# Kernel optimization log

Hardware: AMD Instinct MI355X
Metric: run time of the kernel (lower is better)

The kernel has to match this reference:

```python
import jax, jax.numpy as jnp
import numpy as np

N = 100000      # nodes
E = 1600000     # edges (before self-loops)
F_IN = 16       # num_node_features
HID = 16        # hid
HEADS = 4       # in_head == out_head
B = 64          # num graphs
G = 16          # num_global_features
NEG_SLOPE = 0.2


def gat_conv(x, src, dst, W, a_src, a_dst, b, concat):
    """PyG-style GATConv. x:[N,F], W:[F,H*C], a_src/a_dst:[H,C], b:[H*C] or [C]."""
    n = x.shape[0]
    H, C = a_src.shape
    h = (x @ W).reshape(n, H, C)                       # [N,H,C]
    alpha_s = (h * a_src).sum(-1)                      # [N,H]
    alpha_d = (h * a_dst).sum(-1)                      # [N,H]
    e = jax.nn.leaky_relu(alpha_s[src] + alpha_d[dst], NEG_SLOPE)  # [E',H]
    # segment softmax over destination nodes (stable; max is grad-free)
    m = jax.lax.stop_gradient(jax.ops.segment_max(e, dst, num_segments=n))
    ex = jnp.exp(e - m[dst])
    denom = jax.ops.segment_sum(ex, dst, num_segments=n)
    alpha = ex / (denom[dst] + 1e-16)                  # [E',H]
    out = jax.ops.segment_sum(h[src] * alpha[:, :, None], dst, num_segments=n)  # [N,H,C]
    out = out.reshape(n, H * C) if concat else out.mean(axis=1)
    return out + b


def setup_inputs() -> dict:
    key = jax.random.key(0)
    ks = jax.random.split(key, 24)
    s = 0.1
    inp = {
        "x": jax.random.normal(ks[0], (N, F_IN), jnp.float32),
        "stats": jax.random.normal(ks[1], (B, G), jnp.float32),
        # conv1: F_IN -> HID, heads=HEADS, concat=True
        "W1": jax.random.normal(ks[2], (F_IN, HEADS * HID), jnp.float32) * s,
        "a1s": jax.random.normal(ks[3], (HEADS, HID), jnp.float32) * s,
        "a1d": jax.random.normal(ks[4], (HEADS, HID), jnp.float32) * s,
        "b1": jnp.zeros((HEADS * HID,), jnp.float32),
        # conv2: HID*HEADS -> HID, heads=HEADS, concat=False
        "W2": jax.random.normal(ks[5], (HEADS * HID, HEADS * HID), jnp.float32) * s,
        "a2s": jax.random.normal(ks[6], (HEADS, HID), jnp.float32) * s,
        "a2d": jax.random.normal(ks[7], (HEADS, HID), jnp.float32) * s,
        "b2": jnp.zeros((HID,), jnp.float32),
        # conv3: HID -> HID, heads=HEADS, concat=False
        "W3": jax.random.normal(ks[8], (HID, HEADS * HID), jnp.float32) * s,
        "a3s": jax.random.normal(ks[9], (HEADS, HID), jnp.float32) * s,
        "a3d": jax.random.normal(ks[10], (HEADS, HID), jnp.float32) * s,
        "b3": jnp.zeros((HID,), jnp.float32),
        # MLP head
        "fw1": jax.random.normal(ks[11], (HID + G, 32), jnp.float32) * s,
        "fb1": jnp.zeros((32,), jnp.float32),
        "fw2": jax.random.normal(ks[12], (32, 16), jnp.float32) * s,
        "fb2": jnp.zeros((16,), jnp.float32),
        "fw3": jax.random.normal(ks[13], (16, 1), jnp.float32) * s,
        "fb3": jnp.zeros((1,), jnp.float32),
        "edge_index": jax.random.randint(ks[14], (2, E), 0, N, jnp.int64),
        "batch": jnp.sort(jax.random.randint(ks[15], (N,), 0, B, jnp.int64)),
    }
    return inp


def reference(x, stats, W1, a1s, a1d, b1, W2, a2s, a2d, b2, W3, a3s, a3d, b3,
              fw1, fb1, fw2, fb2, fw3, fb3, edge_index, batch):
    n = x.shape[0]
    loops = jnp.arange(n, dtype=edge_index.dtype)
    src = jnp.concatenate([edge_index[0], loops])  # add_self_loops=True (PyG default)
    dst = jnp.concatenate([edge_index[1], loops])
    h = jax.nn.elu(gat_conv(x, src, dst, W1, a1s, a1d, b1, True))
    h = jax.nn.elu(gat_conv(h, src, dst, W2, a2s, a2d, b2, False))
    h = gat_conv(h, src, dst, W3, a3s, a3d, b3, False)
    nb = stats.shape[0]
    pooled = jax.ops.segment_sum(h, batch, num_segments=nb)
    counts = jax.ops.segment_sum(jnp.ones((n,), h.dtype), batch, num_segments=nb)
    pooled = pooled / jnp.maximum(counts, 1.0)[:, None]   # global_mean_pool
    z = jnp.concatenate([pooled, stats], axis=1)
    z = jax.nn.relu(z @ fw1 + fb1)
    z = jax.nn.relu(z @ fw2 + fb2)
    return z @ fw3 + fb3
```

## Files before the change

kernel.cpp:

```cpp
#include <hip/hip_runtime.h>
#include <hip/hip_bf16.h>
#include <hip/hip_fp16.h>

#define NNODES 100000
#define NEDGES 1600000
#define NHEADS 4
#define NHID   16
#define NB     64
#define NG     16
#define POOL_BLOCKS 256
#define POOL_SLOTS (NB * NG + NB)

#define BKT_SHIFT 7
#define NPB 128
#define NBKT ((NNODES + NPB - 1) / NPB)
#define BCAP 4096
#define SCAT_BLOCKS 256
#define NL1_BLOCKS 2048

typedef float vf2 __attribute__((ext_vector_type(2)));

__device__ __forceinline__ float leaky02(float v) {
    return v > 0.0f ? v : 0.2f * v;
}

__device__ __forceinline__ unsigned char cvt_fp8(float a) {
    int r = __builtin_amdgcn_cvt_pk_fp8_f32(a, a, 0, false);
    return (unsigned char)(r & 0xFF);
}

__device__ __forceinline__ float4 loadQ4(const unsigned char* p) {
    int u = *(const int*)p;
    vf2 lo = __builtin_amdgcn_cvt_pk_f32_fp8(u, false);
    vf2 hi = __builtin_amdgcn_cvt_pk_f32_fp8(u, true);
    return make_float4(lo.x, lo.y, hi.x, hi.y);
}

__device__ __forceinline__ void storeH4(__half* p, float4 v) {
    __half2 a = __floats2half2_rn(v.x, v.y);
    __half2 b = __floats2half2_rn(v.z, v.w);
    uint2 raw;
    raw.x = *reinterpret_cast<unsigned*>(&a);
    raw.y = *reinterpret_cast<unsigned*>(&b);
    *(uint2*)p = raw;
}

template <int FIN>
__device__ __forceinline__ void nl_body_f32(const float* __restrict__ X,
                                            const float* __restrict__ W,
                                            const float* __restrict__ a_s,
                                            const float* __restrict__ a_d,
                                            unsigned char* __restrict__ H,
                                            float* __restrict__ AS,
                                            float* __restrict__ AD, int n,
                                            int wave0, int nwaves, int lane) {
    int head = lane >> 4;
    float w[FIN];
#pragma unroll
    for (int k = 0; k < FIN; ++k) w[k] = W[k * 64 + lane];
    float asl = a_s[lane], adl = a_d[lane];

    for (int i = wave0; i < n; i += nwaves) {
        const float* __restrict__ xr = X + (size_t)i * FIN;
        float acc = 0.0f;
#pragma unroll
        for (int k = 0; k < FIN; ++k) acc += xr[k] * w[k];
        H[(size_t)i * 64 + lane] = cvt_fp8(acc);
        float s1 = acc * asl, s2 = acc * adl;
#pragma unroll
        for (int off = 1; off < 16; off <<= 1) {
            s1 += __shfl_xor(s1, off);
            s2 += __shfl_xor(s2, off);
        }
        if ((lane & 15) == 0) {
            AS[(size_t)i * 4 + head] = s1;
            AD[(size_t)i * 4 + head] = s2;
        }
    }
}

template <int FIN>
__global__ void node_linear3(const float* __restrict__ X,
                             const float* __restrict__ W,
                             const float* __restrict__ a_s,
                             const float* __restrict__ a_d,
                             unsigned char* __restrict__ H,
                             float* __restrict__ AS,
                             float* __restrict__ AD, int n) {
    int lane = threadIdx.x & 63;
    int wave = __builtin_amdgcn_readfirstlane(
        (int)((blockIdx.x * blockDim.x + threadIdx.x) >> 6));
    int nwaves = (gridDim.x * blockDim.x) >> 6;
    nl_body_f32<FIN>(X, W, a_s, a_d, H, AS, AD, n, wave, nwaves, lane);
}

template <int FIN>
__global__ void node_linear3h(const unsigned* __restrict__ X,
                              const float* __restrict__ W,
                              const float* __restrict__ a_s,
                              const float* __restrict__ a_d,
                              unsigned char* __restrict__ H,
                              float* __restrict__ AS,
                              float* __restrict__ AD, int n) {
    int lane = threadIdx.x & 63;
    int head = lane >> 4;
    int wave = __builtin_amdgcn_readfirstlane(
        (int)((blockIdx.x * blockDim.x + threadIdx.x) >> 6));
    int nwaves = (gridDim.x * blockDim.x) >> 6;

    float w[FIN];
#pragma unroll
    for (int k = 0; k < FIN; ++k) w[k] = W[k * 64 + lane];
    float asl = a_s[lane], adl = a_d[lane];

    for (int i = wave; i < n; i += nwaves) {
        const unsigned* __restrict__ xr = X + (size_t)i * (FIN / 2);
        float acc = 0.0f;
#pragma unroll
        for (int k = 0; k < FIN / 2; ++k) {
            unsigned u = xr[k];
            __half2 hh = *reinterpret_cast<const __half2*>(&u);
            float2 f = __half22float2(hh);
            acc += f.x * w[2 * k] + f.y * w[2 * k + 1];
        }
        H[(size_t)i * 64 + lane] = cvt_fp8(acc);
        float s1 = acc * asl, s2 = acc * adl;
#pragma unroll
        for (int off = 1; off < 16; off <<= 1) {
            s1 += __shfl_xor(s1, off);
            s2 += __shfl_xor(s2, off);
        }
        if ((lane & 15) == 0) {
            AS[(size_t)i * 4 + head] = s1;
            AD[(size_t)i * 4 + head] = s2;
        }
    }
}

__global__ void scatter_nl1(const int* __restrict__ src,
                            const int* __restrict__ dst,
                            int* __restrict__ bucketCnt,
                            unsigned int* __restrict__ pairs, int ne,
                            const float* __restrict__ X,
                            const float* __restrict__ W,
                            const float* __restrict__ a_s,
                            const float* __restrict__ a_d,
                            unsigned char* __restrict__ H,
                            float* __restrict__ AS,
                            float* __restrict__ AD, int n) {
    __shared__ int hist[NBKT];
    __shared__ int base[NBKT];
    int tid = threadIdx.x;

    if (blockIdx.x >= SCAT_BLOCKS) {
        int lane = tid & 63;
        int wave = __builtin_amdgcn_readfirstlane(
            (int)(((blockIdx.x - SCAT_BLOCKS) * blockDim.x + tid) >> 6));
        int nwaves = (NL1_BLOCKS * 256) >> 6;
        nl_body_f32<16>(X, W, a_s, a_d, H, AS, AD, n, wave, nwaves, lane);
        return;
    }

    for (int i = tid; i < NBKT; i += 256) hist[i] = 0;
    __syncthreads();

    int chunk = (ne + SCAT_BLOCKS - 1) / SCAT_BLOCKS;
    int beg = blockIdx.x * chunk;
    int end = min(beg + chunk, ne);

    for (int e0 = beg; e0 < end; e0 += 1024) {
        int d[4];
#pragma unroll
        for (int q = 0; q < 4; ++q) {
            int e = e0 + q * 256 + tid;
            d[q] = (e < end) ? dst[e] : -1;
        }
#pragma unroll
        for (int q = 0; q < 4; ++q)
            if (d[q] >= 0) atomicAdd(&hist[d[q] >> BKT_SHIFT], 1);
    }
    __syncthreads();

    for (int i = tid; i < NBKT; i += 256) {
        int h = hist[i];
        base[i] = h ? atomicAdd(&bucketCnt[i], h) : 0;
        hist[i] = 0;
    }
    __syncthreads();

    for (int e0 = beg; e0 < end; e0 += 1024) {
        int d[4], s[4];
#pragma unroll
        for (int q = 0; q < 4; ++q) {
            int e = e0 + q * 256 + tid;
            d[q] = (e < end) ? dst[e] : -1;
            s[q] = (e < end) ? src[e] : 0;
        }
        int r[4], bkt[4];
#pragma unroll
        for (int q = 0; q < 4; ++q) {
            if (d[q] >= 0) {
                bkt[q] = d[q] >> BKT_SHIFT;
                r[q] = base[bkt[q]] + atomicAdd(&hist[bkt[q]], 1);
            }
        }
#pragma unroll
        for (int q = 0; q < 4; ++q) {
            if (d[q] >= 0 && r[q] < BCAP)
                pairs[(size_t)bkt[q] * BCAP + r[q]] =
                    (unsigned)s[q] | ((unsigned)(d[q] & (NPB - 1)) << 20);
        }
    }
}

__global__ void bucket_sort(const unsigned int* __restrict__ pairs,
                            const int* __restrict__ bucketCnt,
                            int* __restrict__ srcs,
                            int* __restrict__ indptr, int n) {
    __shared__ int hist[NPB];
    __shared__ int offl[NPB];
    __shared__ int cur[NPB];
    __shared__ int red[256];
    __shared__ int lsrc[BCAP];
    int bkt = blockIdx.x;
    int t = threadIdx.x;
    int cnt = min(bucketCnt[bkt], BCAP);

    int partial = 0;
    for (int j = t; j < bkt; j += 256) partial += min(bucketCnt[j], BCAP);
    red[t] = partial;
    if (t < NPB) hist[t] = 0;
    __syncthreads();
    for (int s = 128; s > 0; s >>= 1) {
        if (t < s) red[t] += red[t + s];
        __syncthreads();
    }
    int boff = red[0];
    if (bkt == NBKT - 1 && t == 0) indptr[n] = boff + cnt;

    const unsigned int* __restrict__ p = pairs + (size_t)bkt * BCAP;
    unsigned int v[BCAP / 256];
#pragma unroll
    for (int i = 0; i < BCAP / 256; ++i) {
        int e = i * 256 + t;
        v[i] = 0u;
        if (e < cnt) {
            v[i] = p[e];
            atomicAdd(&hist[v[i] >> 20], 1);
        }
    }
    __syncthreads();
    if (t < NPB) offl[t] = hist[t];
    __syncthreads();
    for (int off = 1; off < NPB; off <<= 1) {
        int x = 0;
        if (t < NPB && t >= off) x = offl[t - off];
        __syncthreads();
        if (t < NPB && t >= off) offl[t] += x;
        __syncthreads();
    }
    if (t < NPB) {
        int ex = offl[t] - hist[t];
        cur[t] = ex;
        int node = bkt * NPB + t;
        if (node < n) indptr[node] = boff + ex;
    }
    __syncthreads();
#pragma unroll
    for (int i = 0; i < BCAP / 256; ++i) {
        int e = i * 256 + t;
        if (e < cnt) {
            int r = atomicAdd(&cur[v[i] >> 20], 1);
            lsrc[r] = (int)(v[i] & 0xFFFFFu);
        }
    }
    __syncthreads();
    for (int e = t; e < cnt; e += 256) srcs[boff + e] = lsrc[e];
}

template <int MODE, typename TOUT>
__global__ void gat_pull3(const unsigned char* __restrict__ H,
                          const float* __restrict__ AS,
                          const float* __restrict__ AD,
                          const int* __restrict__ indptr,
                          const int* __restrict__ srcs,
                          const float* __restrict__ bias,
                          TOUT* __restrict__ out, int n) {
    int lane = threadIdx.x & 63;
    int grp  = lane >> 4;
    int sl   = lane & 15;
    int head = sl >> 2;
    int wave = (blockIdx.x * blockDim.x + threadIdx.x) >> 6;
    int nwaves = (gridDim.x * blockDim.x) >> 6;

    for (int d0 = wave * 4; d0 < n; d0 += nwaves * 4) {
        int d = d0 + grp;
        if (d < n) {
            float ad  = AD[(size_t)d * 4 + head];
            float asd = AS[(size_t)d * 4 + head];
            float t0 = asd + ad;
            float wself = __expf(t0 > 0.f ? t0 : 0.2f * t0);
            float den = wself;
            float4 h4s = loadQ4(H + (size_t)d * 64 + sl * 4);
            float4 acc = {wself * h4s.x, wself * h4s.y,
                          wself * h4s.z, wself * h4s.w};

            int beg = indptr[d], end = indptr[d + 1];
            for (int e0 = beg; e0 < end; e0 += 16) {
                int cnt = min(16, end - e0);
                int myS = (sl < cnt) ? srcs[e0 + sl] : 0;
                int j = 0;
                for (; j + 4 <= cnt; j += 4) {
                    int s[4]; float a[4]; float4 h4[4];
#pragma unroll
                    for (int q = 0; q < 4; ++q)
                        s[q] = __shfl(myS, (grp << 4) + j + q);
#pragma unroll
                    for (int q = 0; q < 4; ++q)
                        a[q] = AS[(size_t)s[q] * 4 + head];
#pragma unroll
                    for (int q = 0; q < 4; ++q)
                        h4[q] = loadQ4(H + (size_t)s[q] * 64 + sl * 4);
#pragma unroll
                    for (int q = 0; q < 4; ++q) {
                        float t = a[q] + ad;
                        float w = __expf(t > 0.f ? t : 0.2f * t);
                        den += w;
                        acc.x += w * h4[q].x; acc.y += w * h4[q].y;
                        acc.z += w * h4[q].z; acc.w += w * h4[q].w;
                    }
                }
                for (; j < cnt; ++j) {
                    int s = __shfl(myS, (grp << 4) + j);
                    float t = AS[(size_t)s * 4 + head] + ad;
                    float w = __expf(t > 0.f ? t : 0.2f * t);
                    den += w;
                    float4 h4 = loadQ4(H + (size_t)s * 64 + sl * 4);
                    acc.x += w * h4.x; acc.y += w * h4.y;
                    acc.z += w * h4.z; acc.w += w * h4.w;
                }
            }
            float inv = 1.0f / (den + 1e-16f);
            float4 v = {acc.x * inv, acc.y * inv, acc.z * inv, acc.w * inv};
            if (MODE == 0) {
                float4 b4 = *(const float4*)(bias + sl * 4);
                v.x += b4.x; v.y += b4.y; v.z += b4.z; v.w += b4.w;
                v.x = v.x > 0.f ? v.x : __expf(v.x) - 1.f;
                v.y = v.y > 0.f ? v.y : __expf(v.y) - 1.f;
                v.z = v.z > 0.f ? v.z : __expf(v.z) - 1.f;
                v.w = v.w > 0.f ? v.w : __expf(v.w) - 1.f;
                storeH4((__half*)out + (size_t)d * 64 + sl * 4, v);
            } else {
#pragma unroll
                for (int off = 4; off <= 8; off <<= 1) {
                    v.x += __shfl_xor(v.x, off);
                    v.y += __shfl_xor(v.y, off);
                    v.z += __shfl_xor(v.z, off);
                    v.w += __shfl_xor(v.w, off);
                }
                float4 b4 = *(const float4*)(bias + (sl & 3) * 4);
                v.x = 0.25f * v.x + b4.x; v.y = 0.25f * v.y + b4.y;
                v.z = 0.25f * v.z + b4.z; v.w = 0.25f * v.w + b4.w;
                if (MODE == 1) {
                    v.x = v.x > 0.f ? v.x : __expf(v.x) - 1.f;
                    v.y = v.y > 0.f ? v.y : __expf(v.y) - 1.f;
                    v.z = v.z > 0.f ? v.z : __expf(v.z) - 1.f;
                    v.w = v.w > 0.f ? v.w : __expf(v.w) - 1.f;
                }
                if (sl < 4)
                    *(float4*)((float*)out + (size_t)d * 16 + sl * 4) = v;
            }
        }
    }
}

__global__ void pool_stage1(const float* __restrict__ Hf,
                            const int* __restrict__ batch,
                            float* __restrict__ partials, int n) {
    __shared__ float lp[POOL_SLOTS];
    int tid = threadIdx.x;
    for (int i = tid; i < POOL_SLOTS; i += 256) lp[i] = 0.0f;
    __syncthreads();

    int chunk = (n + POOL_BLOCKS - 1) / POOL_BLOCKS;
    int start = blockIdx.x * chunk;
    int end = min(start + chunk, n);
    int c = tid & 15;
    for (int node = start + (tid >> 4); node < end; node += 16) {
        int b = batch[node];
        atomicAdd(&lp[b * 16 + c], Hf[(size_t)node * 16 + c]);
        if (c == 0) atomicAdd(&lp[NB * NG + b], 1.0f);
    }
    __syncthreads();
    float* outp = partials + (size_t)blockIdx.x * POOL_SLOTS;
    for (int i = tid; i < POOL_SLOTS; i += 256) outp[i] = lp[i];
}

__global__ void pool_stage2(const float* __restrict__ partials,
                            float* __restrict__ pooled_counts) {
    int idx = blockIdx.x * blockDim.x + threadIdx.x;
    if (idx >= POOL_SLOTS) return;
    float s = 0.0f;
    for (int j = 0; j < POOL_BLOCKS; ++j)
        s += partials[(size_t)j * POOL_SLOTS + idx];
    pooled_counts[idx] = s;
}

__global__ void mlp_head(const float* __restrict__ pooled_counts,
                         const float* __restrict__ stats,
                         const float* __restrict__ fw1, const float* __restrict__ fb1,
                         const float* __restrict__ fw2, const float* __restrict__ fb2,
                         const float* __restrict__ fw3, const float* __restrict__ fb3,
                         float* __restrict__ out) {
    int g = threadIdx.x;
    if (g >= NB) return;
    const float* pooled = pooled_counts;
    const float* counts = pooled_counts + NB * NG;
    float z[32];
    float inv = 1.0f / fmaxf(counts[g], 1.0f);
#pragma unroll
    for (int c = 0; c < 16; ++c) z[c] = pooled[g * 16 + c] * inv;
#pragma unroll
    for (int c = 0; c < 16; ++c) z[16 + c] = stats[g * 16 + c];

    float z1[32];
#pragma unroll
    for (int j = 0; j < 32; ++j) {
        float acc = fb1[j];
        for (int k = 0; k < 32; ++k) acc += z[k] * fw1[k * 32 + j];
        z1[j] = fmaxf(acc, 0.0f);
    }
    float z2[16];
#pragma unroll
    for (int j = 0; j < 16; ++j) {
        float acc = fb2[j];
        for (int k = 0; k < 32; ++k) acc += z1[k] * fw2[k * 16 + j];
        z2[j] = fmaxf(acc, 0.0f);
    }
    float acc = fb3[0];
#pragma unroll
    for (int k = 0; k < 16; ++k) acc += z2[k] * fw3[k];
    out[g] = acc;
}

extern "C" void kernel_launch(void* const* d_in, const int* in_sizes, int n_in,
                              void* d_out, int out_size, void* d_ws, size_t ws_size,
                              hipStream_t stream) {
    const float* x    = (const float*)d_in[0];
    const float* stats= (const float*)d_in[1];
    const float* W1   = (const float*)d_in[2];
    const float* a1s  = (const float*)d_in[3];
    const float* a1d  = (const float*)d_in[4];
    const float* b1   = (const float*)d_in[5];
    const float* W2   = (const float*)d_in[6];
    const float* a2s  = (const float*)d_in[7];
    const float* a2d  = (const float*)d_in[8];
    const float* b2   = (const float*)d_in[9];
    const float* W3   = (const float*)d_in[10];
    const float* a3s  = (const float*)d_in[11];
    const float* a3d  = (const float*)d_in[12];
    const float* b3   = (const float*)d_in[13];
    const float* fw1  = (const float*)d_in[14];
    const float* fb1  = (const float*)d_in[15];
    const float* fw2  = (const float*)d_in[16];
    const float* fb2  = (const float*)d_in[17];
    const float* fw3  = (const float*)d_in[18];
    const float* fb3  = (const float*)d_in[19];
    const int* ei     = (const int*)d_in[20];
    const int* batch  = (const int*)d_in[21];

    const int n = NNODES, ne = NEDGES;
    const int* srcI = ei;
    const int* dstI = ei + ne;

    float* ws = (float*)d_ws;
    unsigned char* Hq = (unsigned char*)ws;
    float* B    = (float*)(Hq + (size_t)n * 64);
    __half* B16 = (__half*)B;
    float* C2   = B + (size_t)n * 64;
    float* AS   = C2 + (size_t)n * 16;
    float* AD   = AS + (size_t)n * 4;
    float* PC   = AD + (size_t)n * 4;
    float* PART = PC + POOL_SLOTS;
    int* bucketCnt = (int*)(PART + (size_t)POOL_BLOCKS * POOL_SLOTS);
    int* indptr    = bucketCnt + NBKT;
    int* srcs      = indptr + n + 1;
    unsigned int* pairs = (unsigned int*)B;

    const int TB = 256;
    const int nlBlocks   = 2048;
    const int pullBlocks = (n + 15) / 16;

    hipMemsetAsync(bucketCnt, 0, NBKT * sizeof(int), stream);
    scatter_nl1<<<SCAT_BLOCKS + NL1_BLOCKS, TB, 0, stream>>>(
        srcI, dstI, bucketCnt, pairs, ne,
        x, W1, a1s, a1d, Hq, AS, AD, n);
    bucket_sort<<<NBKT, TB, 0, stream>>>(pairs, bucketCnt, srcs, indptr, n);

    gat_pull3<0, __half><<<pullBlocks, TB, 0, stream>>>(Hq, AS, AD, indptr, srcs, b1, B16, n);

    node_linear3h<64><<<nlBlocks, TB, 0, stream>>>((const unsigned*)B16, W2, a2s, a2d, Hq, AS, AD, n);
    gat_pull3<1, float><<<pullBlocks, TB, 0, stream>>>(Hq, AS, AD, indptr, srcs, b2, C2, n);

    node_linear3<16><<<nlBlocks, TB, 0, stream>>>(C2, W3, a3s, a3d, Hq, AS, AD, n);
    gat_pull3<2, float><<<pullBlocks, TB, 0, stream>>>(Hq, AS, AD, indptr, srcs, b3, B, n);

    pool_stage1<<<POOL_BLOCKS, TB, 0, stream>>>(B, batch, PART, n);
    pool_stage2<<<(POOL_SLOTS + TB - 1) / TB, TB, 0, stream>>>(PART, PC);
    mlp_head<<<1, 64, 0, stream>>>(PC, stats, fw1, fb1, fw2, fb2, fw3, fb3,
                                   (float*)d_out);
}
```

Before: 326.5 us.

## Interleave features with source scores and fuse layer-3 linear and pooling into pulls

Each node's fp8 features and its per-head source attention scores now sit together in one 128-byte record. An edge gather can then fetch both from one cache line instead of two separate arrays. The layer-3 linear transform and its attention scores are computed inside the layer-2 aggregation kernel, with W3 held in LDS, and write to a second record buffer. Global mean pooling is folded into the layer-3 aggregation through LDS atomics followed by global atomics. This removes the node_linear and two pool kernels and their intermediate round trips, at the cost of 128-byte records that carry padding and of global float atomics for pooling.

```diff
diff --git a/kernel.cpp b/kernel.cpp
--- a/kernel.cpp
+++ b/kernel.cpp
@@ -4,11 +4,8 @@
 
 #define NNODES 100000
 #define NEDGES 1600000
-#define NHEADS 4
-#define NHID   16
 #define NB     64
 #define NG     16
-#define POOL_BLOCKS 256
 #define POOL_SLOTS (NB * NG + NB)
 
 #define BKT_SHIFT 7
@@ -17,6 +14,7 @@
 #define BCAP 4096
 #define SCAT_BLOCKS 256
 #define NL1_BLOCKS 2048
+#define REC 128
 
 typedef float vf2 __attribute__((ext_vector_type(2)));
 
@@ -50,8 +48,7 @@
                                             const float* __restrict__ W,
                                             const float* __restrict__ a_s,
                                             const float* __restrict__ a_d,
-                                            unsigned char* __restrict__ H,
-                                            float* __restrict__ AS,
+                                            unsigned char* __restrict__ Hrec,
                                             float* __restrict__ AD, int n,
                                             int wave0, int nwaves, int lane) {
     int head = lane >> 4;
@@ -65,7 +62,8 @@
         float acc = 0.0f;
 #pragma unroll
         for (int k = 0; k < FIN; ++k) acc += xr[k] * w[k];
-        H[(size_t)i * 64 + lane] = cvt_fp8(acc);
+        unsigned char* row = Hrec + (size_t)i * REC;
+        row[lane] = cvt_fp8(acc);
         float s1 = acc * asl, s2 = acc * adl;
 #pragma unroll
         for (int off = 1; off < 16; off <<= 1) {
@@ -73,25 +71,10 @@
             s2 += __shfl_xor(s2, off);
         }
         if ((lane & 15) == 0) {
-            AS[(size_t)i * 4 + head] = s1;
+            ((float*)(row + 64))[head] = s1;
             AD[(size_t)i * 4 + head] = s2;
         }
     }
-}
-
-template <int FIN>
-__global__ void node_linear3(const float* __restrict__ X,
-                             const float* __restrict__ W,
-                             const float* __restrict__ a_s,
-                             const float* __restrict__ a_d,
-                             unsigned char* __restrict__ H,
-                             float* __restrict__ AS,
-                             float* __restrict__ AD, int n) {
-    int lane = threadIdx.x & 63;
-    int wave = __builtin_amdgcn_readfirstlane(
-        (int)((blockIdx.x * blockDim.x + threadIdx.x) >> 6));
-    int nwaves = (gridDim.x * blockDim.x) >> 6;
-    nl_body_f32<FIN>(X, W, a_s, a_d, H, AS, AD, n, wave, nwaves, lane);
 }
 
 template <int FIN>
@@ -99,8 +82,7 @@
                               const float* __restrict__ W,
                               const float* __restrict__ a_s,
                               const float* __restrict__ a_d,
-                              unsigned char* __restrict__ H,
-                              float* __restrict__ AS,
+                              unsigned char* __restrict__ Hrec,
                               float* __restrict__ AD, int n) {
     int lane = threadIdx.x & 63;
     int head = lane >> 4;
@@ -123,7 +105,8 @@
             float2 f = __half22float2(hh);
             acc += f.x * w[2 * k] + f.y * w[2 * k + 1];
         }
-        H[(size_t)i * 64 + lane] = cvt_fp8(acc);
+        unsigned char* row = Hrec + (size_t)i * REC;
+        row[lane] = cvt_fp8(acc);
         float s1 = acc * asl, s2 = acc * adl;
 #pragma unroll
         for (int off = 1; off < 16; off <<= 1) {
@@ -131,7 +114,7 @@
             s2 += __shfl_xor(s2, off);
         }
         if ((lane & 15) == 0) {
-            AS[(size_t)i * 4 + head] = s1;
+            ((float*)(row + 64))[head] = s1;
             AD[(size_t)i * 4 + head] = s2;
         }
     }
@@ -145,8 +128,7 @@
                             const float* __restrict__ W,
                             const float* __restrict__ a_s,
                             const float* __restrict__ a_d,
-                            unsigned char* __restrict__ H,
-                            float* __restrict__ AS,
+                            unsigned char* __restrict__ Hrec,
                             float* __restrict__ AD, int n) {
     __shared__ int hist[NBKT];
     __shared__ int base[NBKT];
@@ -157,7 +139,7 @@
         int wave = __builtin_amdgcn_readfirstlane(
             (int)(((blockIdx.x - SCAT_BLOCKS) * blockDim.x + tid) >> 6));
         int nwaves = (NL1_BLOCKS * 256) >> 6;
-        nl_body_f32<16>(X, W, a_s, a_d, H, AS, AD, n, wave, nwaves, lane);
+        nl_body_f32<16>(X, W, a_s, a_d, Hrec, AD, n, wave, nwaves, lane);
         return;
     }
 
@@ -278,132 +260,203 @@
     for (int e = t; e < cnt; e += 256) srcs[boff + e] = lsrc[e];
 }
 
-template <int MODE, typename TOUT>
-__global__ void gat_pull3(const unsigned char* __restrict__ H,
-                          const float* __restrict__ AS,
-                          const float* __restrict__ AD,
-                          const int* __restrict__ indptr,
-                          const int* __restrict__ srcs,
-                          const float* __restrict__ bias,
-                          TOUT* __restrict__ out, int n) {
+__device__ __forceinline__ float4 gat_agg_core(
+    const unsigned char* __restrict__ Hrec, const float* __restrict__ AD,
+    const int* __restrict__ indptr, const int* __restrict__ srcs,
+    int d, int grp, int sl, int head) {
+    const unsigned char* __restrict__ rowD = Hrec + (size_t)d * REC;
+    float ad  = AD[(size_t)d * 4 + head];
+    float asd = *(const float*)(rowD + 64 + 4 * head);
+    float t0 = asd + ad;
+    float wself = __expf(leaky02(t0));
+    float den = wself;
+    float4 h4s = loadQ4(rowD + sl * 4);
+    float4 acc = make_float4(wself * h4s.x, wself * h4s.y,
+                             wself * h4s.z, wself * h4s.w);
+
+    int beg = indptr[d], end = indptr[d + 1];
+    for (int e0 = beg; e0 < end; e0 += 16) {
+        int cnt = min(16, end - e0);
+        int myS = (sl < cnt) ? srcs[e0 + sl] : 0;
+        int j = 0;
+        for (; j + 4 <= cnt; j += 4) {
+            const unsigned char* r[4];
+            float a[4]; float4 h4[4];
+#pragma unroll
+            for (int q = 0; q < 4; ++q) {
+                int s = __shfl(myS, (grp << 4) + j + q);
+                r[q] = Hrec + (size_t)s * REC;
+            }
+#pragma unroll
+            for (int q = 0; q < 4; ++q)
+                a[q] = *(const float*)(r[q] + 64 + 4 * head);
+#pragma unroll
+            for (int q = 0; q < 4; ++q) h4[q] = loadQ4(r[q] + sl * 4);
+#pragma unroll
+            for (int q = 0; q < 4; ++q) {
+                float t = a[q] + ad;
+                float w = __expf(leaky02(t));
+                den += w;
+                acc.x += w * h4[q].x; acc.y += w * h4[q].y;
+                acc.z += w * h4[q].z; acc.w += w * h4[q].w;
+            }
+        }
+        for (; j < cnt; ++j) {
+            int s = __shfl(myS, (grp << 4) + j);
+            const unsigned char* rr = Hrec + (size_t)s * REC;
+            float t = *(const float*)(rr + 64 + 4 * head) + ad;
+            float w = __expf(leaky02(t));
+            float4 h4 = loadQ4(rr + sl * 4);
+            den += w;
+            acc.x += w * h4.x; acc.y += w * h4.y;
+            acc.z += w * h4.z; acc.w += w * h4.w;
+        }
+    }
+    float inv = 1.0f / (den + 1e-16f);
+    return make_float4(acc.x * inv, acc.y * inv, acc.z * inv, acc.w * inv);
+}
+
+__global__ void gat_pull_l1(const unsigned char* __restrict__ Hrec,
+                            const float* __restrict__ AD,
+                            const int* __restrict__ indptr,
+                            const int* __restrict__ srcs,
+                            const float* __restrict__ bias,
+                            __half* __restrict__ out, int n) {
     int lane = threadIdx.x & 63;
-    int grp  = lane >> 4;
-    int sl   = lane & 15;
-    int head = sl >> 2;
+    int grp = lane >> 4, sl = lane & 15, head = sl >> 2;
     int wave = (blockIdx.x * blockDim.x + threadIdx.x) >> 6;
     int nwaves = (gridDim.x * blockDim.x) >> 6;
-
     for (int d0 = wave * 4; d0 < n; d0 += nwaves * 4) {
         int d = d0 + grp;
         if (d < n) {
-            float ad  = AD[(size_t)d * 4 + head];
-            float asd = AS[(size_t)d * 4 + head];
-            float t0 = asd + ad;
-            float wself = __expf(t0 > 0.f ? t0 : 0.2f * t0);
-            float den = wself;
-            float4 h4s = loadQ4(H + (size_t)d * 64 + sl * 4);
-            float4 acc = {wself * h4s.x, wself * h4s.y,
-                          wself * h4s.z, wself * h4s.w};
-
-            int beg = indptr[d], end = indptr[d + 1];
-            for (int e0 = beg; e0 < end; e0 += 16) {
-                int cnt = min(16, end - e0);
-                int myS = (sl < cnt) ? srcs[e0 + sl] : 0;
-                int j = 0;
-                for (; j + 4 <= cnt; j += 4) {
-                    int s[4]; float a[4]; float4 h4[4];
-#pragma unroll
-                    for (int q = 0; q < 4; ++q)
-                        s[q] = __shfl(myS, (grp << 4) + j + q);
-#pragma unroll
-                    for (int q = 0; q < 4; ++q)
-                        a[q] = AS[(size_t)s[q] * 4 + head];
-#pragma unroll
-                    for (int q = 0; q < 4; ++q)
-                        h4[q] = loadQ4(H + (size_t)s[q] * 64 + sl * 4);
-#pragma unroll
-                    for (int q = 0; q < 4; ++q) {
-                        float t = a[q] + ad;
-                        float w = __expf(t > 0.f ? t : 0.2f * t);
-                        den += w;
-                        acc.x += w * h4[q].x; acc.y += w * h4[q].y;
-                        acc.z += w * h4[q].z; acc.w += w * h4[q].w;
-                    }
-                }
-                for (; j < cnt; ++j) {
-                    int s = __shfl(myS, (grp << 4) + j);
-                    float t = AS[(size_t)s * 4 + head] + ad;
-                    float w = __expf(t > 0.f ? t : 0.2f * t);
-                    den += w;
-                    float4 h4 = loadQ4(H + (size_t)s * 64 + sl * 4);
-                    acc.x += w * h4.x; acc.y += w * h4.y;
-                    acc.z += w * h4.z; acc.w += w * h4.w;
-                }
-            }
-            float inv = 1.0f / (den + 1e-16f);
-            float4 v = {acc.x * inv, acc.y * inv, acc.z * inv, acc.w * inv};
-            if (MODE == 0) {
-                float4 b4 = *(const float4*)(bias + sl * 4);
-                v.x += b4.x; v.y += b4.y; v.z += b4.z; v.w += b4.w;
-                v.x = v.x > 0.f ? v.x : __expf(v.x) - 1.f;
-                v.y = v.y > 0.f ? v.y : __expf(v.y) - 1.f;
-                v.z = v.z > 0.f ? v.z : __expf(v.z) - 1.f;
-                v.w = v.w > 0.f ? v.w : __expf(v.w) - 1.f;
-                storeH4((__half*)out + (size_t)d * 64 + sl * 4, v);
-            } else {
-#pragma unroll
-                for (int off = 4; off <= 8; off <<= 1) {
-                    v.x += __shfl_xor(v.x, off);
-                    v.y += __shfl_xor(v.y, off);
-                    v.z += __shfl_xor(v.z, off);
-                    v.w += __shfl_xor(v.w, off);
-                }
-                float4 b4 = *(const float4*)(bias + (sl & 3) * 4);
-                v.x = 0.25f * v.x + b4.x; v.y = 0.25f * v.y + b4.y;
-                v.z = 0.25f * v.z + b4.z; v.w = 0.25f * v.w + b4.w;
-                if (MODE == 1) {
-                    v.x = v.x > 0.f ? v.x : __expf(v.x) - 1.f;
-                    v.y = v.y > 0.f ? v.y : __expf(v.y) - 1.f;
-                    v.z = v.z > 0.f ? v.z : __expf(v.z) - 1.f;
-                    v.w = v.w > 0.f ? v.w : __expf(v.w) - 1.f;
-                }
-                if (sl < 4)
-                    *(float4*)((float*)out + (size_t)d * 16 + sl * 4) = v;
-            }
-        }
-    }
-}
-
-__global__ void pool_stage1(const float* __restrict__ Hf,
+            float4 v = gat_agg_core(Hrec, AD, indptr, srcs, d, grp, sl, head);
+            float4 b4 = *(const float4*)(bias + sl * 4);
+            v.x += b4.x; v.y += b4.y; v.z += b4.z; v.w += b4.w;
+            v.x = v.x > 0.f ? v.x : __expf(v.x) - 1.f;
+            v.y = v.y > 0.f ? v.y : __expf(v.y) - 1.f;
+            v.z = v.z > 0.f ? v.z : __expf(v.z) - 1.f;
+            v.w = v.w > 0.f ? v.w : __expf(v.w) - 1.f;
+            storeH4(out + (size_t)d * 64 + sl * 4, v);
+        }
+    }
+}
+
+__global__ void gat_pull_l2(const unsigned char* __restrict__ Hrec,
+                            float* __restrict__ AD,
+                            const int* __restrict__ indptr,
+                            const int* __restrict__ srcs,
+                            const float* __restrict__ bias,
+                            const float* __restrict__ W3,
+                            const float* __restrict__ a3s,
+                            const float* __restrict__ a3d,
+                            unsigned char* __restrict__ Hout, int n) {
+    __shared__ float w3s[16 * 64];
+    for (int i = threadIdx.x; i < 16 * 64; i += 256) w3s[i] = W3[i];
+    __syncthreads();
+
+    int lane = threadIdx.x & 63;
+    int grp = lane >> 4, sl = lane & 15, head = sl >> 2;
+    int wave = (blockIdx.x * blockDim.x + threadIdx.x) >> 6;
+    int nwaves = (gridDim.x * blockDim.x) >> 6;
+    float4 as4 = *(const float4*)(a3s + head * 16 + (sl & 3) * 4);
+    float4 ad4 = *(const float4*)(a3d + head * 16 + (sl & 3) * 4);
+    float4 b4  = *(const float4*)(bias + (sl & 3) * 4);
+
+    for (int d0 = wave * 4; d0 < n; d0 += nwaves * 4) {
+        int d = d0 + grp;
+        if (d < n) {
+            float4 v = gat_agg_core(Hrec, AD, indptr, srcs, d, grp, sl, head);
+#pragma unroll
+            for (int off = 4; off <= 8; off <<= 1) {
+                v.x += __shfl_xor(v.x, off);
+                v.y += __shfl_xor(v.y, off);
+                v.z += __shfl_xor(v.z, off);
+                v.w += __shfl_xor(v.w, off);
+            }
+            v.x = 0.25f * v.x + b4.x; v.y = 0.25f * v.y + b4.y;
+            v.z = 0.25f * v.z + b4.z; v.w = 0.25f * v.w + b4.w;
+            v.x = v.x > 0.f ? v.x : __expf(v.x) - 1.f;
+            v.y = v.y > 0.f ? v.y : __expf(v.y) - 1.f;
+            v.z = v.z > 0.f ? v.z : __expf(v.z) - 1.f;
+            v.w = v.w > 0.f ? v.w : __expf(v.w) - 1.f;
+
+            float xin[16];
+#pragma unroll
+            for (int q = 0; q < 4; ++q) {
+                int srcl = (grp << 4) + q;
+                xin[4 * q + 0] = __shfl(v.x, srcl);
+                xin[4 * q + 1] = __shfl(v.y, srcl);
+                xin[4 * q + 2] = __shfl(v.z, srcl);
+                xin[4 * q + 3] = __shfl(v.w, srcl);
+            }
+            float4 o = make_float4(0.f, 0.f, 0.f, 0.f);
+#pragma unroll
+            for (int k = 0; k < 16; ++k) {
+                float4 wr = *(const float4*)&w3s[k * 64 + 4 * sl];
+                o.x += xin[k] * wr.x; o.y += xin[k] * wr.y;
+                o.z += xin[k] * wr.z; o.w += xin[k] * wr.w;
+            }
+            unsigned char* rowO = Hout + (size_t)d * REC;
+            int pk = __builtin_amdgcn_cvt_pk_fp8_f32(o.x, o.y, 0, false);
+            pk = __builtin_amdgcn_cvt_pk_fp8_f32(o.z, o.w, pk, true);
+            *(int*)(rowO + 4 * sl) = pk;
+            float s1 = o.x * as4.x + o.y * as4.y + o.z * as4.z + o.w * as4.w;
+            float s2 = o.x * ad4.x + o.y * ad4.y + o.z * ad4.z + o.w * ad4.w;
+            s1 += __shfl_xor(s1, 1); s1 += __shfl_xor(s1, 2);
+            s2 += __shfl_xor(s2, 1); s2 += __shfl_xor(s2, 2);
+            if ((sl & 3) == 0) {
+                ((float*)(rowO + 64))[head] = s1;
+                AD[(size_t)d * 4 + head] = s2;
+            }
+        }
+    }
+}
+
+__global__ void gat_pull_l3(const unsigned char* __restrict__ Hrec,
+                            const float* __restrict__ AD,
+                            const int* __restrict__ indptr,
+                            const int* __restrict__ srcs,
+                            const float* __restrict__ bias,
                             const int* __restrict__ batch,
-                            float* __restrict__ partials, int n) {
+                            float* __restrict__ PC, int n) {
     __shared__ float lp[POOL_SLOTS];
-    int tid = threadIdx.x;
-    for (int i = tid; i < POOL_SLOTS; i += 256) lp[i] = 0.0f;
-    __syncthreads();
-
-    int chunk = (n + POOL_BLOCKS - 1) / POOL_BLOCKS;
-    int start = blockIdx.x * chunk;
-    int end = min(start + chunk, n);
-    int c = tid & 15;
-    for (int node = start + (tid >> 4); node < end; node += 16) {
-        int b = batch[node];
-        atomicAdd(&lp[b * 16 + c], Hf[(size_t)node * 16 + c]);
-        if (c == 0) atomicAdd(&lp[NB * NG + b], 1.0f);
-    }
-    __syncthreads();
-    float* outp = partials + (size_t)blockIdx.x * POOL_SLOTS;
-    for (int i = tid; i < POOL_SLOTS; i += 256) outp[i] = lp[i];
-}
-
-__global__ void pool_stage2(const float* __restrict__ partials,
-                            float* __restrict__ pooled_counts) {
-    int idx = blockIdx.x * blockDim.x + threadIdx.x;
-    if (idx >= POOL_SLOTS) return;
-    float s = 0.0f;
-    for (int j = 0; j < POOL_BLOCKS; ++j)
-        s += partials[(size_t)j * POOL_SLOTS + idx];
-    pooled_counts[idx] = s;
+    for (int i = threadIdx.x; i < POOL_SLOTS; i += 256) lp[i] = 0.f;
+    __syncthreads();
+
+    int lane = threadIdx.x & 63;
+    int grp = lane >> 4, sl = lane & 15, head = sl >> 2;
+    int wave = (blockIdx.x * blockDim.x + threadIdx.x) >> 6;
+    int nwaves = (gridDim.x * blockDim.x) >> 6;
+    float4 b4 = *(const float4*)(bias + (sl & 3) * 4);
+
+    for (int d0 = wave * 4; d0 < n; d0 += nwaves * 4) {
+        int d = d0 + grp;
+        if (d < n) {
+            float4 v = gat_agg_core(Hrec, AD, indptr, srcs, d, grp, sl, head);
+#pragma unroll
+            for (int off = 4; off <= 8; off <<= 1) {
+                v.x += __shfl_xor(v.x, off);
+                v.y += __shfl_xor(v.y, off);
+                v.z += __shfl_xor(v.z, off);
+                v.w += __shfl_xor(v.w, off);
+            }
+            v.x = 0.25f * v.x + b4.x; v.y = 0.25f * v.y + b4.y;
+            v.z = 0.25f * v.z + b4.z; v.w = 0.25f * v.w + b4.w;
+            if (sl < 4) {
+                int b = batch[d];
+                atomicAdd(&lp[b * 16 + sl * 4 + 0], v.x);
+                atomicAdd(&lp[b * 16 + sl * 4 + 1], v.y);
+                atomicAdd(&lp[b * 16 + sl * 4 + 2], v.z);
+                atomicAdd(&lp[b * 16 + sl * 4 + 3], v.w);
+                if (sl == 0) atomicAdd(&lp[NB * NG + b], 1.0f);
+            }
+        }
+    }
+    __syncthreads();
+    for (int i = threadIdx.x; i < POOL_SLOTS; i += 256) {
+        float s = lp[i];
+        if (s != 0.f) atomicAdd(&PC[i], s);
+    }
 }
 
 __global__ void mlp_head(const float* __restrict__ pooled_counts,
@@ -473,40 +526,38 @@
     const int* srcI = ei;
     const int* dstI = ei + ne;
 
-    float* ws = (float*)d_ws;
-    unsigned char* Hq = (unsigned char*)ws;
-    float* B    = (float*)(Hq + (size_t)n * 64);
-    __half* B16 = (__half*)B;
-    float* C2   = B + (size_t)n * 64;
-    float* AS   = C2 + (size_t)n * 16;
-    float* AD   = AS + (size_t)n * 4;
+    unsigned char* HqA = (unsigned char*)d_ws;
+    unsigned char* HqB = HqA + (size_t)n * REC;
+    float* AD   = (float*)(HqB + (size_t)n * REC);
     float* PC   = AD + (size_t)n * 4;
-    float* PART = PC + POOL_SLOTS;
-    int* bucketCnt = (int*)(PART + (size_t)POOL_BLOCKS * POOL_SLOTS);
+    int* bucketCnt = (int*)(PC + POOL_SLOTS);
     int* indptr    = bucketCnt + NBKT;
-    int* srcs      = indptr + n + 1;
-    unsigned int* pairs = (unsigned int*)B;
+    int* srcs      = indptr + (n + 1);
+    size_t off = (size_t)((char*)(srcs + ne) - (char*)d_ws);
+    off = (off + 255) & ~(size_t)255;
+    unsigned int* pairs = (unsigned int*)((char*)d_ws + off);
+    __half* B16 = (__half*)pairs;
 
     const int TB = 256;
     const int nlBlocks   = 2048;
     const int pullBlocks = (n + 15) / 16;
 
-    hipMemsetAsync(bucketCnt, 0, NBKT * sizeof(int), stream);
+    hipMemsetAsync(PC, 0, (POOL_SLOTS + NBKT) * sizeof(int), stream);
+
     scatter_nl1<<<SCAT_BLOCKS + NL1_BLOCKS, TB, 0, stream>>>(
         srcI, dstI, bucketCnt, pairs, ne,
-        x, W1, a1s, a1d, Hq, AS, AD, n);
+        x, W1, a1s, a1d, HqA, AD, n);
     bucket_sort<<<NBKT, TB, 0, stream>>>(pairs, bucketCnt, srcs, indptr, n);
 
-    gat_pull3<0, __half><<<pullBlocks, TB, 0, stream>>>(Hq, AS, AD, indptr, srcs, b1, B16, n);
-
-    node_linear3h<64><<<nlBlocks, TB, 0, stream>>>((const unsigned*)B16, W2, a2s, a2d, Hq, AS, AD, n);
-    gat_pull3<1, float><<<pullBlocks, TB, 0, stream>>>(Hq, AS, AD, indptr, srcs, b2, C2, n);
-
-    node_linear3<16><<<nlBlocks, TB, 0, stream>>>(C2, W3, a3s, a3d, Hq, AS, AD, n);
-    gat_pull3<2, float><<<pullBlocks, TB, 0, stream>>>(Hq, AS, AD, indptr, srcs, b3, B, n);
-
-    pool_stage1<<<POOL_BLOCKS, TB, 0, stream>>>(B, batch, PART, n);
-    pool_stage2<<<(POOL_SLOTS + TB - 1) / TB, TB, 0, stream>>>(PART, PC);
+    gat_pull_l1<<<pullBlocks, TB, 0, stream>>>(HqA, AD, indptr, srcs, b1, B16, n);
+
+    node_linear3h<64><<<nlBlocks, TB, 0, stream>>>((const unsigned*)B16, W2,
+                                                   a2s, a2d, HqA, AD, n);
+    gat_pull_l2<<<pullBlocks, TB, 0, stream>>>(HqA, AD, indptr, srcs, b2,
+                                               W3, a3s, a3d, HqB, n);
+    gat_pull_l3<<<pullBlocks, TB, 0, stream>>>(HqB, AD, indptr, srcs, b3,
+                                               batch, PC, n);
+
     mlp_head<<<1, 64, 0, stream>>>(PC, stats, fw1, fb1, fw2, fb2, fw3, fb3,
                                    (float*)d_out);
 }
```

Measured after the change: 331.1 us. No clear change (+1.4%).
